# Optimization experiments

Hardware: AMD Instinct MI355X
Metric: run time of the kernel (lower is better)

Reference implementation:

```python
import jax, jax.numpy as jnp
import numpy as np

N, E, D_IN, HID, HEADS, D_OUT, R = 20000, 640000, 256, 128, 4, 128, 32
NEG_SLOPE = 0.2  # PyG GATConv default


def setup_inputs() -> dict:
    key = jax.random.key(0)
    ks = jax.random.split(key, 12)
    s = 0.05
    return {
        "x": jax.random.normal(ks[0], (N, D_IN), jnp.float32),
        "edge_index": jax.random.randint(ks[1], (2, E), 0, N, dtype=jnp.int64),
        "edge_type": jax.random.randint(ks[2], (E,), 0, R, dtype=jnp.int64),
        "rel_emb": jax.random.normal(ks[3], (R, D_IN), jnp.float32) * s,
        "W1": jax.random.normal(ks[4], (D_IN, HEADS * HID), jnp.float32) * s,
        "att_src1": jax.random.normal(ks[5], (HEADS, HID), jnp.float32) * s,
        "att_dst1": jax.random.normal(ks[6], (HEADS, HID), jnp.float32) * s,
        "b1": jnp.zeros((HEADS * HID,), jnp.float32),
        "W2": jax.random.normal(ks[7], (HEADS * HID, D_OUT), jnp.float32) * s,
        "att_src2": jax.random.normal(ks[8], (1, D_OUT), jnp.float32) * s,
        "att_dst2": jax.random.normal(ks[9], (1, D_OUT), jnp.float32) * s,
        "b2": jnp.zeros((D_OUT,), jnp.float32),
    }


def _gat_conv(x, src, dst, W, a_src, a_dst, bias, heads, ch):
    """PyG GATConv (eval mode, self loops already in src/dst)."""
    n = x.shape[0]
    h = (x @ W).reshape(n, heads, ch)                      # [N,H,C]
    alpha_s = jnp.einsum('nhc,hc->nh', h, a_src)           # [N,H]
    alpha_d = jnp.einsum('nhc,hc->nh', h, a_dst)
    e = jax.nn.leaky_relu(alpha_s[src] + alpha_d[dst], NEG_SLOPE)  # [E,H]
    # segment softmax over incoming edges of each dst node
    m = jax.ops.segment_max(e, dst, num_segments=n)        # [N,H]
    p = jnp.exp(e - m[dst])
    denom = jax.ops.segment_sum(p, dst, num_segments=n)
    alpha = p / (denom[dst] + 1e-16)                       # [E,H]
    out = jax.ops.segment_sum(h[src] * alpha[:, :, None], dst, num_segments=n)
    return out.reshape(n, heads * ch) + bias


def reference(x, edge_index, edge_type, rel_emb, W1, att_src1, att_dst1, b1,
              W2, att_src2, att_dst2, b2):
    src, dst = edge_index[0], edge_index[1]
    # relational feature injection: x_mod[src] += rel_emb[edge_type]
    x_mod = x.at[src].add(rel_emb[edge_type])
    # GATConv adds self loops by default
    loop = jnp.arange(N, dtype=src.dtype)
    s2 = jnp.concatenate([src, loop])
    d2 = jnp.concatenate([dst, loop])
    h = _gat_conv(x_mod, s2, d2, W1, att_src1, att_dst1, b1, HEADS, HID)
    h = jax.nn.elu(h)
    return _gat_conv(h, s2, d2, W2, att_src2, att_dst2, b2, 1, D_OUT)
```

## Files before the change

### kernel.cpp

```cpp
#include <hip/hip_runtime.h>


#define D_IN   256
#define HID1   512
#define NHEADS 4
#define DOUT   128
#define NREL   32
#define NEG_SLOPE 0.2f
#define M_PAD  20096
#define NB     128

static __device__ __forceinline__ unsigned short f2b(float f) {
  union { float f; unsigned int i; } v; v.f = f;
  unsigned int x = v.i;
  return (unsigned short)((x + 0x7fffu + ((x >> 16) & 1u)) >> 16);
}
static __device__ __forceinline__ float lrelu(float x) {
  return x > 0.f ? x : NEG_SLOPE * x;
}

typedef __attribute__((ext_vector_type(8))) short bf16x8;
typedef __attribute__((ext_vector_type(4))) float f32x4;
typedef __attribute__((ext_vector_type(2))) float f32x2;
typedef __attribute__((ext_vector_type(2))) unsigned int u32x2;

static __device__ __forceinline__ f32x2 up2(unsigned int u) {
  union { unsigned int i; float f; } lo, hi;
  lo.i = u << 16; hi.i = u & 0xffff0000u;
  f32x2 v; v.x = lo.f; v.y = hi.f; return v;
}
static __device__ __forceinline__ void pkfma(f32x2& a, f32x2 b, f32x2 c) {
  asm("v_pk_fma_f32 %0, %1, %2, %0" : "+v"(a) : "v"(b), "v"(c));
}
static __device__ __forceinline__ void accp(f32x2* acc, float w, uint4 r) {
  f32x2 wv = (f32x2)(w);
  pkfma(acc[0], wv, up2(r.x));
  pkfma(acc[1], wv, up2(r.y));
  pkfma(acc[2], wv, up2(r.z));
  pkfma(acc[3], wv, up2(r.w));
}

__global__ __launch_bounds__(256) void hist_prep_kernel(
    const int* __restrict__ src, const int* __restrict__ dst,
    const int* __restrict__ et, unsigned int* __restrict__ counts8,
    int* __restrict__ gtable, int E, int n, int cb,
    const float* __restrict__ W1, const float* __restrict__ W2,
    unsigned short* __restrict__ W1T, unsigned short* __restrict__ W2T,
    const float* __restrict__ att_s1, const float* __restrict__ att_d1,
    float* __restrict__ us4, float* __restrict__ ud4,
    const float* __restrict__ att_s2, const float* __restrict__ att_d2,
    float* __restrict__ vs, float* __restrict__ vd) {
  int b = blockIdx.x;
  int t = threadIdx.x;
  if (b < NB) {
    extern __shared__ int hist[];
    for (int i = t; i < n; i += 256) hist[i] = 0;
    __syncthreads();
    int per = (E + NB - 1) / NB;
    int e0 = b * per;
    int e1 = min(e0 + per, E);
    for (int e = e0 + t; e < e1; e += 256) {
      atomicAdd(&hist[dst[e]], 1);
      int s = src[e], r = et[e];
      atomicAdd(&counts8[(size_t)s * 8 + (r >> 2)], 1u << (8 * (r & 3)));
    }
    __syncthreads();
    for (int i = t; i < n; i += 256) gtable[(size_t)b * n + i] = hist[i];
  } else if (b < NB + cb) {
    int idx = (b - NB) * 256 + t;
    if (idx < D_IN * HID1) {
      int r = idx / HID1, c = idx % HID1;
      W1T[(size_t)c * D_IN + r] = f2b(W1[idx]);
    } else {
      int k = idx - D_IN * HID1;
      if (k < HID1 * DOUT) {
        int r = k / DOUT, c = k % DOUT;
        W2T[(size_t)c * HID1 + r] = f2b(W2[k]);
      }
    }
  } else if (b == NB + cb) {
    int k = t;
    float us[4] = {0.f, 0.f, 0.f, 0.f}, ud[4] = {0.f, 0.f, 0.f, 0.f};
    for (int h = 0; h < 4; ++h)
      for (int c = 0; c < 128; ++c) {
        float wv = W1[(size_t)k * HID1 + h * 128 + c];
        us[h] += wv * att_s1[h * 128 + c];
        ud[h] += wv * att_d1[h * 128 + c];
      }
    ((float4*)us4)[k] = make_float4(us[0], us[1], us[2], us[3]);
    ((float4*)ud4)[k] = make_float4(ud[0], ud[1], ud[2], ud[3]);
  } else {
#pragma unroll
    for (int rr = 0; rr < 2; ++rr) {
      int r = t * 2 + rr;
      float ss = 0.f, dd = 0.f;
      for (int c = 0; c < DOUT; ++c) {
        float wv = W2[(size_t)r * DOUT + c];
        ss += wv * att_s2[c];
        dd += wv * att_d2[c];
      }
      vs[r] = ss; vd[r] = dd;
    }
  }
}

__global__ void colsum_kernel(const int* __restrict__ gtable,
                              int* __restrict__ deg, int n) {
  int d = blockIdx.x * 256 + threadIdx.x;
  if (d >= n) return;
  int s = 0;
#pragma unroll 8
  for (int b = 0; b < NB; ++b) s += gtable[(size_t)b * n + d];
  deg[d] = s;
}

__global__ void scan_local(const int* __restrict__ in, int* __restrict__ out,
                           int* __restrict__ bsum, int n) {
  __shared__ int wsum[4];
  int t = threadIdx.x;
  int base = blockIdx.x * 1024 + t * 4;
  int v0 = (base + 0 < n) ? in[base + 0] : 0;
  int v1 = (base + 1 < n) ? in[base + 1] : 0;
  int v2 = (base + 2 < n) ? in[base + 2] : 0;
  int v3 = (base + 3 < n) ? in[base + 3] : 0;
  int s = v0 + v1 + v2 + v3;
  int lane = t & 63, w = t >> 6;
  int sc = s;
  for (int off = 1; off < 64; off <<= 1) {
    int u = __shfl_up(sc, off);
    if (lane >= off) sc += u;
  }
  if (lane == 63) wsum[w] = sc;
  __syncthreads();
  int woff = 0;
  for (int i = 0; i < w; ++i) woff += wsum[i];
  int excl = woff + sc - s;
  if (base + 0 < n) out[base + 0] = excl;
  if (base + 1 < n) out[base + 1] = excl + v0;
  if (base + 2 < n) out[base + 2] = excl + v0 + v1;
  if (base + 3 < n) out[base + 3] = excl + v0 + v1 + v2;
  if (t == 255) bsum[blockIdx.x] = woff + sc;
}

__global__ void scan_blocks(int* __restrict__ bsum, int nb,
                            int* __restrict__ offsets, int n) {
  int t = threadIdx.x;
  int v = (t < nb) ? bsum[t] : 0;
  int sc = v;
  for (int off = 1; off < 64; off <<= 1) {
    int u = __shfl_up(sc, off);
    if (t >= off) sc += u;
  }
  if (t < nb) bsum[t] = sc - v;
  if (t == nb - 1) offsets[n] = v;
}

__global__ void rebase_kernel(int* __restrict__ gtable,
                              const int* __restrict__ offsets,
                              const int* __restrict__ bsum, int n) {
  int d = blockIdx.x * 256 + threadIdx.x;
  if (d >= n) return;
  int run = offsets[d] + bsum[d >> 10];
  for (int b = 0; b < NB; ++b) {
    size_t idx = (size_t)b * n + d;
    int v = gtable[idx];
    gtable[idx] = run;
    run += v;
  }
}

__global__ __launch_bounds__(256) void scatter2_kernel(
    const int* __restrict__ src, const int* __restrict__ dst,
    const int* __restrict__ gtable, int* __restrict__ csr_src, int E, int n) {
  extern __shared__ int cur[];
  int b = blockIdx.x;
  int t = threadIdx.x;
  for (int i = t; i < n; i += 256) cur[i] = gtable[(size_t)b * n + i];
  __syncthreads();
  int per = (E + NB - 1) / NB;
  int e0 = b * per;
  int e1 = min(e0 + per, E);
  for (int e = e0 + t; e < e1; e += 256) {
    int pos = atomicAdd(&cur[dst[e]], 1);
    csr_src[pos] = src[e];
  }
}

__global__ __launch_bounds__(256) void xmod_kernel(
    const float* __restrict__ x, const unsigned int* __restrict__ counts8,
    const float* __restrict__ rel, const float* __restrict__ us4,
    const float* __restrict__ ud4, unsigned short* __restrict__ x_modb,
    float* __restrict__ as1, float* __restrict__ ad1, int n_nodes) {
  int wv = threadIdx.x >> 6;
  int node = blockIdx.x * 4 + wv;
  if (node >= n_nodes) return;
  int l = threadIdx.x & 63;
  int r5 = l & 31;
  unsigned int cw = counts8[(size_t)node * 8 + (r5 >> 2)];
  int cnt_l = (int)((cw >> (8 * (r5 & 3))) & 0xffu);
  const float4* x4 = (const float4*)x;
  const float4* rel4 = (const float4*)rel;
  float4 v = x4[(size_t)node * 64 + l];
#pragma unroll
  for (int r = 0; r < NREL; ++r) {
    int c = __shfl(cnt_l, r);
    if (c) {
      float4 rv = rel4[r * 64 + l];
      float fc = (float)c;
      v.x += fc * rv.x; v.y += fc * rv.y; v.z += fc * rv.z; v.w += fc * rv.w;
    }
  }
  ushort4 o;
  o.x = f2b(v.x); o.y = f2b(v.y); o.z = f2b(v.z); o.w = f2b(v.w);
  *(ushort4*)(x_modb + (size_t)node * D_IN + l * 4) = o;
  const float4* usv = (const float4*)us4;
  const float4* udv = (const float4*)ud4;
  float vv[4] = {v.x, v.y, v.z, v.w};
  float sh[4] = {0.f, 0.f, 0.f, 0.f}, dh[4] = {0.f, 0.f, 0.f, 0.f};
#pragma unroll
  for (int i = 0; i < 4; ++i) {
    float4 uu = usv[l * 4 + i];
    float4 dd = udv[l * 4 + i];
    sh[0] += vv[i] * uu.x; sh[1] += vv[i] * uu.y; sh[2] += vv[i] * uu.z; sh[3] += vv[i] * uu.w;
    dh[0] += vv[i] * dd.x; dh[1] += vv[i] * dd.y; dh[2] += vv[i] * dd.z; dh[3] += vv[i] * dd.w;
  }
  for (int off = 32; off; off >>= 1) {
#pragma unroll
    for (int h = 0; h < 4; ++h) {
      sh[h] += __shfl_xor(sh[h], off);
      dh[h] += __shfl_xor(dh[h], off);
    }
  }
  if (l == 0) {
    ((float4*)as1)[node] = make_float4(sh[0], sh[1], sh[2], sh[3]);
    ((float4*)ad1)[node] = make_float4(dh[0], dh[1], dh[2], dh[3]);
  }
}

__global__ __launch_bounds__(192) void aggregate1_kernel(
    const unsigned short* __restrict__ x_modb,
    const float* __restrict__ as1, const float* __restrict__ ad1,
    const int* __restrict__ offsets, const int* __restrict__ bsum,
    const int* __restrict__ csr_src,
    unsigned short* __restrict__ agg_xb, int n_nodes) {
  __shared__ __align__(16) unsigned short buf[3][8192 + 512];
  int wid = threadIdx.x >> 6;
  int node = blockIdx.x * 3 + wid;
  if (node >= n_nodes) return;
  int lane = threadIdx.x & 63;
  int l32 = lane & 31;
  unsigned short* rowbuf = &buf[wid][0];
  unsigned short* wbuf = &buf[wid][8192];
  int lo = offsets[node] + bsum[node >> 10];
  int hi = offsets[node + 1] + bsum[(node + 1) >> 10];
  int nchunk = (hi - lo + 32) >> 5;
  float4 adv = ((const float4*)ad1)[node];
  float4 asp = ((const float4*)as1)[node];

  unsigned trbase =
      (unsigned)(size_t)(__attribute__((address_space(3))) unsigned short*)rowbuf +
      (unsigned)((lane >> 4) * 256 + (lane & 15) * 8);

  f32x4 acc[16];
#pragma unroll
  for (int s = 0; s < 16; ++s) acc[s] = (f32x4)(0.f);
  float den0 = 0.f, den1 = 0.f, den2 = 0.f, den3 = 0.f;

  for (int c = 0; c < nchunk; ++c) {
    int q = lo + c * 32 + l32;
    int srcn = (q < hi) ? csr_src[q] : node;
    int sst = __shfl(srcn, lane >> 1);
    const unsigned short* gp = x_modb + (size_t)sst * D_IN + (lane & 1) * 8;
#pragma unroll
    for (int s = 0; s < 16; ++s)
      __builtin_amdgcn_global_load_lds(
          (const __attribute__((address_space(1))) void*)(gp + s * 16),
          (__attribute__((address_space(3))) void*)(rowbuf + s * 512), 16, 0, 0);
    float4 av = (q < hi) ? ((const float4*)as1)[srcn] : asp;
    bool val = q <= hi;
    float w0 = val ? __expf(lrelu(av.x + adv.x)) : 0.f;
    float w1 = val ? __expf(lrelu(av.y + adv.y)) : 0.f;
    float w2 = val ? __expf(lrelu(av.z + adv.z)) : 0.f;
    float w3 = val ? __expf(lrelu(av.w + adv.w)) : 0.f;
    unsigned short h0 = f2b(w0), h1 = f2b(w1), h2 = f2b(w2), h3 = f2b(w3);
    union { unsigned u; float f; } rr;
    rr.u = (unsigned)h0 << 16; float r0 = rr.f;
    rr.u = (unsigned)h1 << 16; float r1 = rr.f;
    rr.u = (unsigned)h2 << 16; float r2 = rr.f;
    rr.u = (unsigned)h3 << 16; float r3 = rr.f;
#pragma unroll
    for (int off = 16; off; off >>= 1) {
      r0 += __shfl_xor(r0, off);
      r1 += __shfl_xor(r1, off);
      r2 += __shfl_xor(r2, off);
      r3 += __shfl_xor(r3, off);
    }
    den0 += r0; den1 += r1; den2 += r2; den3 += r3;
    if (lane < 32) {
      wbuf[0 * 32 + l32] = h0;
      wbuf[1 * 32 + l32] = h1;
      wbuf[2 * 32 + l32] = h2;
      wbuf[3 * 32 + l32] = h3;
    }
    bf16x8 afrag = *(const bf16x8*)(wbuf + (lane & 15) * 32 + (lane >> 4) * 8);
    asm volatile("s_waitcnt vmcnt(0)" ::: "memory");
#pragma unroll
    for (int g = 0; g < 2; ++g) {
      u32x2 t[16];
#pragma unroll
      for (int s = 0; s < 8; ++s) {
        asm volatile("ds_read_b64_tr_b16 %0, %1 offset:%2"
                     : "=v"(t[2 * s]) : "v"(trbase), "i"(g * 8192 + s * 1024));
        asm volatile("ds_read_b64_tr_b16 %0, %1 offset:%2"
                     : "=v"(t[2 * s + 1]) : "v"(trbase), "i"(g * 8192 + s * 1024 + 128));
      }
      asm volatile("s_waitcnt lgkmcnt(0)" ::: "memory");
      __builtin_amdgcn_sched_barrier(0);
#pragma unroll
      for (int s = 0; s < 8; ++s) {
        union { u32x2 h[2]; bf16x8 v; } bb;
        bb.h[0] = t[2 * s]; bb.h[1] = t[2 * s + 1];
        acc[g * 8 + s] =
            __builtin_amdgcn_mfma_f32_16x16x32_bf16(afrag, bb.v, acc[g * 8 + s], 0, 0, 0);
      }
    }
  }
  float i0 = 1.f / (den0 + 1e-16f);
  float i1 = 1.f / (den1 + 1e-16f);
  float i2 = 1.f / (den2 + 1e-16f);
  float i3 = 1.f / (den3 + 1e-16f);
  if (lane < 16) {
#pragma unroll
    for (int s = 0; s < 16; ++s) {
      agg_xb[((size_t)0 * M_PAD + node) * D_IN + s * 16 + lane] = f2b(acc[s][0] * i0);
      agg_xb[((size_t)1 * M_PAD + node) * D_IN + s * 16 + lane] = f2b(acc[s][1] * i1);
      agg_xb[((size_t)2 * M_PAD + node) * D_IN + s * 16 + lane] = f2b(acc[s][2] * i2);
      agg_xb[((size_t)3 * M_PAD + node) * D_IN + s * 16 + lane] = f2b(acc[s][3] * i3);
    }
  }
}

template <int BM, int MODE>
__global__ __launch_bounds__(256) void mfma_gemm(
    const unsigned short* __restrict__ A, const unsigned short* __restrict__ BT,
    unsigned short* __restrict__ C, int M, int N, int K,
    const float* __restrict__ bias, const float* __restrict__ vs,
    const float* __restrict__ vd, float* __restrict__ as2, float* __restrict__ ad2) {
  constexpr int MFR = BM / 32;
  __shared__ __align__(16) unsigned short Asl[BM * 32];
  __shared__ __align__(16) unsigned short Bsl[128 * 32];
  int tid = threadIdx.x;
  int m0 = blockIdx.y * BM, n0 = blockIdx.x * 128;
  int lane = tid & 63, wv = tid >> 6;
  int wm = wv & 1, wn = wv >> 1;
  int l16 = lane & 15, quad = lane >> 4;
  int lr = lane >> 2, lseg = lane & 3;
  if (MODE == 1) A += (size_t)blockIdx.x * M_PAD * K;

  f32x4 acc[MFR][4];
#pragma unroll
  for (int i = 0; i < MFR; ++i)
#pragma unroll
    for (int j = 0; j < 4; ++j) acc[i][j] = (f32x4)(0.f);

  for (int k0 = 0; k0 < K; k0 += 32) {
#pragma unroll
    for (int c = wv; c < BM / 16; c += 4) {
      int gr = m0 + c * 16 + lr; gr = gr < M ? gr : M - 1;
      __builtin_amdgcn_global_load_lds(
          (const __attribute__((address_space(1))) void*)(A + (size_t)gr * K + k0 + lseg * 8),
          (__attribute__((address_space(3))) void*)(&Asl[c * 512]), 16, 0, 0);
    }
#pragma unroll
    for (int c = wv; c < 8; c += 4) {
      int gr = n0 + c * 16 + lr;
      __builtin_amdgcn_global_load_lds(
          (const __attribute__((address_space(1))) void*)(BT + (size_t)gr * K + k0 + lseg * 8),
          (__attribute__((address_space(3))) void*)(&Bsl[c * 512]), 16, 0, 0);
    }
    __syncthreads();
    bf16x8 af[MFR], bfr[4];
#pragma unroll
    for (int mf = 0; mf < MFR; ++mf)
      af[mf] = *(const bf16x8*)(&Asl[(wm * (BM / 2) + mf * 16 + l16) * 32 + quad * 8]);
#pragma unroll
    for (int nf = 0; nf < 4; ++nf)
      bfr[nf] = *(const bf16x8*)(&Bsl[(wn * 64 + nf * 16 + l16) * 32 + quad * 8]);
#pragma unroll
    for (int mf = 0; mf < MFR; ++mf)
#pragma unroll
      for (int nf = 0; nf < 4; ++nf)
        acc[mf][nf] = __builtin_amdgcn_mfma_f32_16x16x32_bf16(af[mf], bfr[nf], acc[mf][nf], 0, 0, 0);
    __syncthreads();
  }
  if (MODE == 0) {
#pragma unroll
    for (int mf = 0; mf < MFR; ++mf)
#pragma unroll
      for (int nf = 0; nf < 4; ++nf)
#pragma unroll
        for (int r = 0; r < 4; ++r) {
          int row = m0 + wm * (BM / 2) + mf * 16 + quad * 4 + r;
          int col = n0 + wn * 64 + nf * 16 + l16;
          C[(size_t)row * N + col] = f2b(acc[mf][nf][r]);
        }
  } else {
#pragma unroll
    for (int mf = 0; mf < MFR; ++mf)
#pragma unroll
      for (int r = 0; r < 4; ++r) {
        int row = m0 + wm * (BM / 2) + mf * 16 + quad * 4 + r;
        float sd = 0.f, dd = 0.f;
#pragma unroll
        for (int nf = 0; nf < 4; ++nf) {
          int col = n0 + wn * 64 + nf * 16 + l16;
          float cv = acc[mf][nf][r] + bias[col];
          cv = cv > 0.f ? cv : expm1f(cv);
          C[(size_t)row * N + col] = f2b(cv);
          sd += cv * vs[col];
          dd += cv * vd[col];
        }
#pragma unroll
        for (int off = 1; off < 16; off <<= 1) {
          sd += __shfl_xor(sd, off);
          dd += __shfl_xor(dd, off);
        }
        if (l16 == 0 && row < M) {
          atomicAdd(&as2[row], sd);
          atomicAdd(&ad2[row], dd);
        }
      }
  }
}

__global__ __launch_bounds__(256) void aggregate2_kernel(
    const unsigned short* __restrict__ t2b,
    const float* __restrict__ as2, const float* __restrict__ ad2,
    const int* __restrict__ offsets, const int* __restrict__ bsum,
    const int* __restrict__ csr_src,
    const float* __restrict__ bias, float* __restrict__ out, int n_nodes) {
  int node = blockIdx.x * 4 + (threadIdx.x >> 6);
  if (node >= n_nodes) return;
  int lane = threadIdx.x & 63;
  int g = lane >> 4, l16 = lane & 15;
  int lo = offsets[node] + bsum[node >> 10];
  int hi = offsets[node + 1] + bsum[(node + 1) >> 10];
  float ad = ad2[node];

  const uint4* t2v = (const uint4*)t2b;
  f32x2 acc[4];
#pragma unroll
  for (int k = 0; k < 4; ++k) acc[k] = (f32x2)(0.f);
  float denom = 0.f;
  int nit = (hi - lo + 3) >> 2;
  int j = lo + g;
  bool valid = j < hi;
  int s = valid ? csr_src[j] : node;
  float asv = as2[s];
  uint4 tv = t2v[(unsigned)((s << 4) | l16)];
  for (int i = 0; i < nit; ++i) {
    int jn = j + 4;
    bool vn = jn < hi;
    int sn = vn ? csr_src[jn] : node;
    float asv_n = as2[sn];
    uint4 tvn = t2v[(unsigned)((sn << 4) | l16)];
    float w = valid ? __expf(lrelu(asv + ad)) : 0.f;
    accp(acc, w, tv);
    denom += w;
    j = jn; valid = vn; s = sn; asv = asv_n; tv = tvn;
  }
  if (g == 0) {
    uint4 tv2 = t2v[(unsigned)((node << 4) | l16)];
    float w = __expf(lrelu(as2[node] + ad));
    accp(acc, w, tv2);
    denom += w;
  }
#pragma unroll
  for (int k = 0; k < 4; ++k) {
    acc[k].x += __shfl_xor(acc[k].x, 16); acc[k].y += __shfl_xor(acc[k].y, 16);
    acc[k].x += __shfl_xor(acc[k].x, 32); acc[k].y += __shfl_xor(acc[k].y, 32);
  }
  denom += __shfl_xor(denom, 16);
  denom += __shfl_xor(denom, 32);
  if (g == 0) {
    float inv = 1.f / (denom + 1e-16f);
    float4 o0, o1;
    o0.x = acc[0].x * inv + bias[l16 * 8 + 0];
    o0.y = acc[0].y * inv + bias[l16 * 8 + 1];
    o0.z = acc[1].x * inv + bias[l16 * 8 + 2];
    o0.w = acc[1].y * inv + bias[l16 * 8 + 3];
    o1.x = acc[2].x * inv + bias[l16 * 8 + 4];
    o1.y = acc[2].y * inv + bias[l16 * 8 + 5];
    o1.z = acc[3].x * inv + bias[l16 * 8 + 6];
    o1.w = acc[3].y * inv + bias[l16 * 8 + 7];
    *(float4*)(out + (size_t)node * DOUT + l16 * 8) = o0;
    *(float4*)(out + (size_t)node * DOUT + l16 * 8 + 4) = o1;
  }
}

extern "C" void kernel_launch(void* const* d_in, const int* in_sizes, int n_in,
                              void* d_out, int out_size, void* d_ws, size_t ws_size,
                              hipStream_t stream) {
  const float* x     = (const float*)d_in[0];
  const int* ei      = (const int*)d_in[1];
  const int* etype   = (const int*)d_in[2];
  const float* rel   = (const float*)d_in[3];
  const float* W1    = (const float*)d_in[4];
  const float* at_s1 = (const float*)d_in[5];
  const float* at_d1 = (const float*)d_in[6];
  const float* b1    = (const float*)d_in[7];
  const float* W2    = (const float*)d_in[8];
  const float* at_s2 = (const float*)d_in[9];
  const float* at_d2 = (const float*)d_in[10];
  const float* b2v   = (const float*)d_in[11];
  float* out         = (float*)d_out;

  const int N = in_sizes[0] / D_IN;
  const int E = in_sizes[2];
  const int* srcv = ei;
  const int* dstv = ei + E;

  char* p = (char*)d_ws;
  auto carve = [&](size_t bytes) -> char* {
    char* r = p; p += (bytes + 255) & ~(size_t)255; return r;
  };
  unsigned int* counts8 = (unsigned int*)carve((size_t)N * 8 * 4);
  float* as2     = (float*)carve((size_t)N * 4);
  float* ad2     = (float*)carve((size_t)N * 4);
  size_t zero_bytes = (size_t)(p - (char*)counts8);
  int*   deg     = (int*)carve((size_t)N * 4);
  int*   offsets = (int*)carve(((size_t)N + 1) * 4);
  int*   bsum    = (int*)carve(64 * 4);
  float* as1     = (float*)carve((size_t)N * NHEADS * 4);
  float* ad1     = (float*)carve((size_t)N * NHEADS * 4);
  float* vs      = (float*)carve((size_t)HID1 * 4);
  float* vd      = (float*)carve((size_t)HID1 * 4);
  float* us4     = (float*)carve((size_t)D_IN * 4 * 4);
  float* ud4     = (float*)carve((size_t)D_IN * 4 * 4);
  int*   csr_src = (int*)carve((size_t)E * 4);
  unsigned short* W1T    = (unsigned short*)carve((size_t)HID1 * D_IN * 2);
  unsigned short* W2T    = (unsigned short*)carve((size_t)DOUT * HID1 * 2);
  unsigned short* x_modb = (unsigned short*)carve((size_t)N * D_IN * 2);
  unsigned short* agg_xb = (unsigned short*)carve((size_t)NHEADS * M_PAD * D_IN * 2);
  unsigned short* h2b    = (unsigned short*)carve((size_t)M_PAD * HID1 * 2);
  unsigned short* t2b    = (unsigned short*)carve((size_t)M_PAD * DOUT * 2);
  int* gtable = (int*)h2b;

  hipMemsetAsync(counts8, 0, zero_bytes, stream);

  int cb = (D_IN * HID1 + HID1 * DOUT + 255) / 256;
  int nb = (N + 1023) / 1024;
  int ldsb = N * 4;
  hist_prep_kernel<<<NB + cb + 2, 256, ldsb, stream>>>(
      srcv, dstv, etype, counts8, gtable, E, N, cb,
      W1, W2, W1T, W2T, at_s1, at_d1, us4, ud4, at_s2, at_d2, vs, vd);
  colsum_kernel<<<(N + 255) / 256, 256, 0, stream>>>(gtable, deg, N);
  scan_local<<<nb, 256, 0, stream>>>(deg, offsets, bsum, N);
  scan_blocks<<<1, 64, 0, stream>>>(bsum, nb, offsets, N);
  rebase_kernel<<<(N + 255) / 256, 256, 0, stream>>>(gtable, offsets, bsum, N);
  scatter2_kernel<<<NB, 256, ldsb, stream>>>(srcv, dstv, gtable, csr_src, E, N);
  xmod_kernel<<<(N + 3) / 4, 256, 0, stream>>>(x, counts8, rel, us4, ud4, x_modb, as1, ad1, N);
  aggregate1_kernel<<<(N + 2) / 3, 192, 0, stream>>>(x_modb, as1, ad1, offsets, bsum,
                                                     csr_src, agg_xb, N);
  mfma_gemm<128, 1><<<dim3(NHEADS, M_PAD / 128), 256, 0, stream>>>(
      agg_xb, W1T, h2b, N, HID1, D_IN, b1, vs, vd, as2, ad2);
  mfma_gemm<64, 0><<<dim3(DOUT / 128, M_PAD / 64), 256, 0, stream>>>(
      h2b, W2T, t2b, N, DOUT, HID1, nullptr, nullptr, nullptr, nullptr, nullptr);
  aggregate2_kernel<<<(N + 3) / 4, 256, 0, stream>>>(
      t2b, as2, ad2, offsets, bsum, csr_src, b2v, out, N);
}
```

Measured before the change: 315.5 us.

## Split aggregate1 node across four waves with double-buffered chunk prefetch

Rewrites the first-layer aggregation so each 256-thread block handles one destination node. Each of its four waves owns a quarter of the feature columns, instead of one wave per node handling all 256 columns. The neighbor rows and softmax weights of the next 32-edge chunk are prefetched into a second LDS buffer while MFMAs run on the current chunk. The denominator is reduced once at the end instead of per chunk. This cuts per-wave register and accumulator load and hides gather latency, at the cost of a block-wide barrier per chunk and more, smaller blocks.

```diff
diff --git a/kernel.cpp b/kernel.cpp
--- a/kernel.cpp
+++ b/kernel.cpp
@@ -14,6 +14,9 @@
   union { float f; unsigned int i; } v; v.f = f;
   unsigned int x = v.i;
   return (unsigned short)((x + 0x7fffu + ((x >> 16) & 1u)) >> 16);
+}
+static __device__ __forceinline__ float b2f(unsigned short h) {
+  union { unsigned int i; float f; } v; v.i = (unsigned int)h << 16; return v.f;
 }
 static __device__ __forceinline__ float lrelu(float x) {
   return x > 0.f ? x : NEG_SLOPE * x;
@@ -237,105 +240,162 @@
   }
 }
 
-__global__ __launch_bounds__(192) void aggregate1_kernel(
+__global__ __launch_bounds__(256) void aggregate1_kernel(
     const unsigned short* __restrict__ x_modb,
     const float* __restrict__ as1, const float* __restrict__ ad1,
     const int* __restrict__ offsets, const int* __restrict__ bsum,
     const int* __restrict__ csr_src,
     unsigned short* __restrict__ agg_xb, int n_nodes) {
-  __shared__ __align__(16) unsigned short buf[3][8192 + 512];
-  int wid = threadIdx.x >> 6;
-  int node = blockIdx.x * 3 + wid;
-  if (node >= n_nodes) return;
-  int lane = threadIdx.x & 63;
-  int l32 = lane & 31;
-  unsigned short* rowbuf = &buf[wid][0];
-  unsigned short* wbuf = &buf[wid][8192];
+  __shared__ __align__(16) unsigned short rowbuf[2][8192];
+  __shared__ __align__(16) unsigned short wtile[2][512];
+  __shared__ float invs[4];
+  int node = blockIdx.x;
+  int tid = threadIdx.x;
+  int w = tid >> 6, lane = tid & 63;
+  int l32 = lane & 31, g = lane >> 4, n16 = lane & 15;
   int lo = offsets[node] + bsum[node >> 10];
   int hi = offsets[node + 1] + bsum[(node + 1) >> 10];
   int nchunk = (hi - lo + 32) >> 5;
-  float4 adv = ((const float4*)ad1)[node];
-  float4 asp = ((const float4*)as1)[node];
-
-  unsigned trbase =
-      (unsigned)(size_t)(__attribute__((address_space(3))) unsigned short*)rowbuf +
-      (unsigned)((lane >> 4) * 256 + (lane & 15) * 8);
-
-  f32x4 acc[16];
-#pragma unroll
-  for (int s = 0; s < 16; ++s) acc[s] = (f32x4)(0.f);
+
+  for (int idx = tid; idx < 2 * 384; idx += 256)
+    wtile[idx >> 8 >> 1 ? 1 : idx / 384][128 + (idx % 384)] = 0;
+
+  const float4* as1v = (const float4*)as1;
+  float4 adv = make_float4(0.f, 0.f, 0.f, 0.f);
+  if (w == 0) adv = ((const float4*)ad1)[node];
+
+  unsigned trl =
+      (unsigned)(size_t)(__attribute__((address_space(3))) unsigned short*)&rowbuf[0][0] +
+      (unsigned)(g * 256 + n16 * 8 + w * 4096);
+
+  f32x4 acc[4];
+#pragma unroll
+  for (int i = 0; i < 4; ++i) acc[i] = (f32x4)(0.f);
   float den0 = 0.f, den1 = 0.f, den2 = 0.f, den3 = 0.f;
 
+  int q0 = lo + l32;
+  int s_cur = (q0 < hi) ? csr_src[q0] : node;
+  {
+    int sst = __shfl(s_cur, lane >> 1);
+    const unsigned short* gp = x_modb + (size_t)sst * D_IN + (lane & 1) * 8;
+#pragma unroll
+    for (int i = 0; i < 4; ++i) {
+      int S = 4 * w + i;
+      __builtin_amdgcn_global_load_lds(
+          (const __attribute__((address_space(1))) void*)(gp + S * 16),
+          (__attribute__((address_space(3))) void*)(&rowbuf[0][S * 512]), 16, 0, 0);
+    }
+  }
+  int s_nxt = 0;
+  if (nchunk > 1) {
+    int q1 = lo + 32 + l32;
+    s_nxt = (q1 < hi) ? csr_src[q1] : node;
+  }
+  if (w == 0) {
+    float4 av = as1v[(unsigned)s_cur];
+    bool val = q0 <= hi;
+    float e0 = val ? __expf(lrelu(av.x + adv.x)) : 0.f;
+    float e1 = val ? __expf(lrelu(av.y + adv.y)) : 0.f;
+    float e2 = val ? __expf(lrelu(av.z + adv.z)) : 0.f;
+    float e3 = val ? __expf(lrelu(av.w + adv.w)) : 0.f;
+    unsigned short h0 = f2b(e0), h1 = f2b(e1), h2 = f2b(e2), h3 = f2b(e3);
+    den0 += b2f(h0); den1 += b2f(h1); den2 += b2f(h2); den3 += b2f(h3);
+    if (lane < 32) {
+      wtile[0][0 * 32 + l32] = h0;
+      wtile[0][1 * 32 + l32] = h1;
+      wtile[0][2 * 32 + l32] = h2;
+      wtile[0][3 * 32 + l32] = h3;
+    }
+  }
+  asm volatile("s_waitcnt vmcnt(0)" ::: "memory");
+  __syncthreads();
+
   for (int c = 0; c < nchunk; ++c) {
-    int q = lo + c * 32 + l32;
-    int srcn = (q < hi) ? csr_src[q] : node;
-    int sst = __shfl(srcn, lane >> 1);
-    const unsigned short* gp = x_modb + (size_t)sst * D_IN + (lane & 1) * 8;
-#pragma unroll
-    for (int s = 0; s < 16; ++s)
-      __builtin_amdgcn_global_load_lds(
-          (const __attribute__((address_space(1))) void*)(gp + s * 16),
-          (__attribute__((address_space(3))) void*)(rowbuf + s * 512), 16, 0, 0);
-    float4 av = (q < hi) ? ((const float4*)as1)[srcn] : asp;
-    bool val = q <= hi;
-    float w0 = val ? __expf(lrelu(av.x + adv.x)) : 0.f;
-    float w1 = val ? __expf(lrelu(av.y + adv.y)) : 0.f;
-    float w2 = val ? __expf(lrelu(av.z + adv.z)) : 0.f;
-    float w3 = val ? __expf(lrelu(av.w + adv.w)) : 0.f;
-    unsigned short h0 = f2b(w0), h1 = f2b(w1), h2 = f2b(w2), h3 = f2b(w3);
-    union { unsigned u; float f; } rr;
-    rr.u = (unsigned)h0 << 16; float r0 = rr.f;
-    rr.u = (unsigned)h1 << 16; float r1 = rr.f;
-    rr.u = (unsigned)h2 << 16; float r2 = rr.f;
-    rr.u = (unsigned)h3 << 16; float r3 = rr.f;
-#pragma unroll
-    for (int off = 16; off; off >>= 1) {
-      r0 += __shfl_xor(r0, off);
-      r1 += __shfl_xor(r1, off);
-      r2 += __shfl_xor(r2, off);
-      r3 += __shfl_xor(r3, off);
-    }
-    den0 += r0; den1 += r1; den2 += r2; den3 += r3;
-    if (lane < 32) {
-      wbuf[0 * 32 + l32] = h0;
-      wbuf[1 * 32 + l32] = h1;
-      wbuf[2 * 32 + l32] = h2;
-      wbuf[3 * 32 + l32] = h3;
-    }
-    bf16x8 afrag = *(const bf16x8*)(wbuf + (lane & 15) * 32 + (lane >> 4) * 8);
-    asm volatile("s_waitcnt vmcnt(0)" ::: "memory");
-#pragma unroll
-    for (int g = 0; g < 2; ++g) {
-      u32x2 t[16];
-#pragma unroll
-      for (int s = 0; s < 8; ++s) {
+    int cb = c & 1, nb2 = cb ^ 1;
+    bool more = (c + 1) < nchunk;
+    int s_c1 = s_nxt;
+    float4 avn = make_float4(0.f, 0.f, 0.f, 0.f);
+    if (more) {
+      int sst = __shfl(s_c1, lane >> 1);
+      const unsigned short* gp = x_modb + (size_t)sst * D_IN + (lane & 1) * 8;
+#pragma unroll
+      for (int i = 0; i < 4; ++i) {
+        int S = 4 * w + i;
+        __builtin_amdgcn_global_load_lds(
+            (const __attribute__((address_space(1))) void*)(gp + S * 16),
+            (__attribute__((address_space(3))) void*)(&rowbuf[nb2][S * 512]), 16, 0, 0);
+      }
+      if (w == 0) avn = as1v[(unsigned)s_c1];
+      if (c + 2 < nchunk) {
+        int q2 = lo + (c + 2) * 32 + l32;
+        s_nxt = (q2 < hi) ? csr_src[q2] : node;
+      }
+    }
+    {
+      unsigned trb = trl + (unsigned)(cb * 16384);
+      bf16x8 afrag = *(const bf16x8*)(&wtile[cb][n16 * 32 + g * 8]);
+      u32x2 t[8];
+#pragma unroll
+      for (int i = 0; i < 4; ++i) {
         asm volatile("ds_read_b64_tr_b16 %0, %1 offset:%2"
-                     : "=v"(t[2 * s]) : "v"(trbase), "i"(g * 8192 + s * 1024));
+                     : "=v"(t[2 * i]) : "v"(trb), "i"(i * 1024));
         asm volatile("ds_read_b64_tr_b16 %0, %1 offset:%2"
-                     : "=v"(t[2 * s + 1]) : "v"(trbase), "i"(g * 8192 + s * 1024 + 128));
+                     : "=v"(t[2 * i + 1]) : "v"(trb), "i"(i * 1024 + 128));
       }
       asm volatile("s_waitcnt lgkmcnt(0)" ::: "memory");
       __builtin_amdgcn_sched_barrier(0);
 #pragma unroll
-      for (int s = 0; s < 8; ++s) {
+      for (int i = 0; i < 4; ++i) {
         union { u32x2 h[2]; bf16x8 v; } bb;
-        bb.h[0] = t[2 * s]; bb.h[1] = t[2 * s + 1];
-        acc[g * 8 + s] =
-            __builtin_amdgcn_mfma_f32_16x16x32_bf16(afrag, bb.v, acc[g * 8 + s], 0, 0, 0);
-      }
-    }
-  }
-  float i0 = 1.f / (den0 + 1e-16f);
-  float i1 = 1.f / (den1 + 1e-16f);
-  float i2 = 1.f / (den2 + 1e-16f);
-  float i3 = 1.f / (den3 + 1e-16f);
+        bb.h[0] = t[2 * i]; bb.h[1] = t[2 * i + 1];
+        acc[i] = __builtin_amdgcn_mfma_f32_16x16x32_bf16(afrag, bb.v, acc[i], 0, 0, 0);
+      }
+    }
+    if (more && w == 0) {
+      int qn = lo + (c + 1) * 32 + l32;
+      bool val = qn <= hi;
+      float e0 = val ? __expf(lrelu(avn.x + adv.x)) : 0.f;
+      float e1 = val ? __expf(lrelu(avn.y + adv.y)) : 0.f;
+      float e2 = val ? __expf(lrelu(avn.z + adv.z)) : 0.f;
+      float e3 = val ? __expf(lrelu(avn.w + adv.w)) : 0.f;
+      unsigned short h0 = f2b(e0), h1 = f2b(e1), h2 = f2b(e2), h3 = f2b(e3);
+      den0 += b2f(h0); den1 += b2f(h1); den2 += b2f(h2); den3 += b2f(h3);
+      if (lane < 32) {
+        wtile[nb2][0 * 32 + l32] = h0;
+        wtile[nb2][1 * 32 + l32] = h1;
+        wtile[nb2][2 * 32 + l32] = h2;
+        wtile[nb2][3 * 32 + l32] = h3;
+      }
+    }
+    asm volatile("s_waitcnt vmcnt(0)" ::: "memory");
+    __syncthreads();
+  }
+
+  if (w == 0) {
+#pragma unroll
+    for (int off = 16; off; off >>= 1) {
+      den0 += __shfl_xor(den0, off);
+      den1 += __shfl_xor(den1, off);
+      den2 += __shfl_xor(den2, off);
+      den3 += __shfl_xor(den3, off);
+    }
+    if (lane == 0) {
+      invs[0] = 1.f / (den0 + 1e-16f);
+      invs[1] = 1.f / (den1 + 1e-16f);
+      invs[2] = 1.f / (den2 + 1e-16f);
+      invs[3] = 1.f / (den3 + 1e-16f);
+    }
+  }
+  __syncthreads();
+  float i0 = invs[0], i1 = invs[1], i2 = invs[2], i3 = invs[3];
   if (lane < 16) {
 #pragma unroll
-    for (int s = 0; s < 16; ++s) {
-      agg_xb[((size_t)0 * M_PAD + node) * D_IN + s * 16 + lane] = f2b(acc[s][0] * i0);
-      agg_xb[((size_t)1 * M_PAD + node) * D_IN + s * 16 + lane] = f2b(acc[s][1] * i1);
-      agg_xb[((size_t)2 * M_PAD + node) * D_IN + s * 16 + lane] = f2b(acc[s][2] * i2);
-      agg_xb[((size_t)3 * M_PAD + node) * D_IN + s * 16 + lane] = f2b(acc[s][3] * i3);
+    for (int i = 0; i < 4; ++i) {
+      int S = 4 * w + i;
+      agg_xb[((size_t)0 * M_PAD + node) * D_IN + S * 16 + lane] = f2b(acc[i][0] * i0);
+      agg_xb[((size_t)1 * M_PAD + node) * D_IN + S * 16 + lane] = f2b(acc[i][1] * i1);
+      agg_xb[((size_t)2 * M_PAD + node) * D_IN + S * 16 + lane] = f2b(acc[i][2] * i2);
+      agg_xb[((size_t)3 * M_PAD + node) * D_IN + S * 16 + lane] = f2b(acc[i][3] * i3);
     }
   }
 }
@@ -560,8 +620,8 @@
   rebase_kernel<<<(N + 255) / 256, 256, 0, stream>>>(gtable, offsets, bsum, N);
   scatter2_kernel<<<NB, 256, ldsb, stream>>>(srcv, dstv, gtable, csr_src, E, N);
   xmod_kernel<<<(N + 3) / 4, 256, 0, stream>>>(x, counts8, rel, us4, ud4, x_modb, as1, ad1, N);
-  aggregate1_kernel<<<(N + 2) / 3, 192, 0, stream>>>(x_modb, as1, ad1, offsets, bsum,
-                                                     csr_src, agg_xb, N);
+  aggregate1_kernel<<<N, 256, 0, stream>>>(x_modb, as1, ad1, offsets, bsum,
+                                           csr_src, agg_xb, N);
   mfma_gemm<128, 1><<<dim3(NHEADS, M_PAD / 128), 256, 0, stream>>>(
       agg_xb, W1T, h2b, N, HID1, D_IN, b1, vs, vd, as2, ad2);
   mfma_gemm<64, 0><<<dim3(DOUT / 128, M_PAD / 64), 256, 0, stream>>>(
```

Result: slower. 323.8 us (+2.7%).
